# Optimization experiments

Measured on AMD Instinct MI355X. Metric: run time of the kernel, lower is better.

## Reference

```python
import jax, jax.numpy as jnp
import numpy as np

N_NODES = 100000
N_EDGES = 1000000
D_FEAT = 64


def setup_inputs() -> dict:
    key = jax.random.key(0)
    ks = jax.random.split(key, 8)
    X = jax.random.normal(ks[0], (N_NODES, D_FEAT), dtype=jnp.float32)
    ref_a = jax.random.randint(ks[1], (N_EDGES,), 0, N_NODES, dtype=jnp.int32)
    ref_b = jax.random.randint(ks[2], (N_EDGES,), 0, N_NODES, dtype=jnp.int32)
    v_map = jax.random.randint(ks[3], (N_NODES,), 0, 128, dtype=jnp.int32)
    v_count = jax.random.randint(ks[4], (128,), 0, 1000, dtype=jnp.int32)
    # Glorot-uniform weights per build()
    lim = float(np.sqrt(6.0 / (D_FEAT + D_FEAT)))
    W_hidden = jax.random.uniform(ks[5], (D_FEAT, D_FEAT), jnp.float32, -lim, lim)
    W_out = jax.random.uniform(ks[6], (D_FEAT, D_FEAT), jnp.float32, -lim, lim)
    b_hidden = jnp.zeros((D_FEAT,), jnp.float32)
    b_out = jnp.zeros((D_FEAT,), jnp.float32)
    return {
        "X": X, "ref_a": ref_a, "ref_b": ref_b, "v_map": v_map, "v_count": v_count,
        "W_hidden": W_hidden, "b_hidden": b_hidden, "W_out": W_out, "b_out": b_out,
    }


def reference(X, ref_a, ref_b, v_map, v_count, W_hidden, b_hidden, W_out, b_out):
    # gin_convolution_compact: GIN aggregation with eps=0 over a compact
    # (undirected, stored-once) edge list: X_agg[v] = X[v] + sum_{u in N(v)} X[u]
    X_agg = X.at[ref_a].add(X[ref_b])
    X_agg = X_agg.at[ref_b].add(X[ref_a])
    # 2-layer MLP with relu after each layer
    X_hid = jax.nn.relu(X_agg @ W_hidden + b_hidden)
    X_out = jax.nn.relu(X_hid @ W_out + b_out)
    return X_out
```

## Files before the change

### kernel.cpp

```cpp
#include <hip/hip_runtime.h>

#define D_FEAT 64
#define BUK_SHIFT 9
#define NPBUK 512
#define MAX_BUK 256
#define SRC_BITS 20
#define SRC_MASK 0xFFFFFu
#define CHUNK_E 8192
#define MAX_BUK_RECS 16384

__global__ __launch_bounds__(256) void bucket_count_kernel(
    const int* __restrict__ ref_a, const int* __restrict__ ref_b,
    int* __restrict__ buk_cnt, int n_edges) {
    __shared__ int hist[MAX_BUK];
    hist[threadIdx.x] = 0;
    __syncthreads();
    int stride = gridDim.x * blockDim.x;
    for (int e = blockIdx.x * blockDim.x + threadIdx.x; e < n_edges; e += stride) {
        atomicAdd(&hist[ref_a[e] >> BUK_SHIFT], 1);
        atomicAdd(&hist[ref_b[e] >> BUK_SHIFT], 1);
    }
    __syncthreads();
    int c = hist[threadIdx.x];
    if (c) atomicAdd(&buk_cnt[threadIdx.x], c);
}

__global__ void bucket_scan_kernel(int* __restrict__ bs, int* __restrict__ cursor,
                                   int* __restrict__ row_start, int n_nodes) {
    int lane = threadIdx.x;
    int carry = 0;
    for (int base = 0; base < MAX_BUK; base += 64) {
        int i = base + lane;
        int v = bs[i];
        int inc = v;
        #pragma unroll
        for (int d = 1; d < 64; d <<= 1) {
            int t = __shfl_up(inc, d);
            if (lane >= d) inc += t;
        }
        int excl = carry + inc - v;
        bs[i] = excl;
        cursor[i] = excl;
        carry += __shfl(inc, 63);
    }
    if (lane == 0) {
        bs[MAX_BUK] = carry;
        row_start[n_nodes] = carry;
    }
}

__global__ __launch_bounds__(256) void bucket_scatter_kernel(
    const int* __restrict__ ref_a, const int* __restrict__ ref_b,
    int* __restrict__ gcur, unsigned* __restrict__ recs, int n_edges) {
    __shared__ int cnt[MAX_BUK];
    __shared__ int base[MAX_BUK];
    __shared__ int cur[MAX_BUK];
    int tid = threadIdx.x;
    int e0 = blockIdx.x * CHUNK_E;
    int e1 = min(e0 + CHUNK_E, n_edges);

    cnt[tid] = 0;
    __syncthreads();
    for (int e = e0 + tid; e < e1; e += 256) {
        atomicAdd(&cnt[ref_a[e] >> BUK_SHIFT], 1);
        atomicAdd(&cnt[ref_b[e] >> BUK_SHIFT], 1);
    }
    __syncthreads();
    int c = cnt[tid];
    base[tid] = c ? atomicAdd(&gcur[tid], c) : 0;
    cur[tid] = 0;
    __syncthreads();
    for (int e = e0 + tid; e < e1; e += 256) {
        int a = ref_a[e];
        int b = ref_b[e];
        int ba = a >> BUK_SHIFT;
        int pa = base[ba] + atomicAdd(&cur[ba], 1);
        recs[pa] = ((unsigned)(a & (NPBUK - 1)) << SRC_BITS) | (unsigned)b;
        int bb = b >> BUK_SHIFT;
        int pb = base[bb] + atomicAdd(&cur[bb], 1);
        recs[pb] = ((unsigned)(b & (NPBUK - 1)) << SRC_BITS) | (unsigned)a;
    }
}

__global__ __launch_bounds__(256) void bucket_sort_kernel(
    const int* __restrict__ bucket_start,
    unsigned* __restrict__ recs,
    int* __restrict__ row_start, int n_nodes) {
    __shared__ unsigned buf[MAX_BUK_RECS];
    __shared__ int cnt[NPBUK];
    __shared__ int lcur[NPBUK];
    int buk = blockIdx.x;
    int tid = threadIdx.x;
    int s = bucket_start[buk];
    int n = bucket_start[buk + 1] - s;
    for (int i = tid; i < NPBUK; i += 256) cnt[i] = 0;
    __syncthreads();
    for (int i = tid; i < n; i += 256) {
        unsigned r = recs[s + i];
        buf[i] = r;
        atomicAdd(&cnt[r >> SRC_BITS], 1);
    }
    __syncthreads();
    if (tid < 64) {
        int lane = tid;
        int carry = 0;
        for (int b2 = 0; b2 < NPBUK; b2 += 64) {
            int i = b2 + lane;
            int v = cnt[i];
            int inc = v;
            #pragma unroll
            for (int d = 1; d < 64; d <<= 1) {
                int t = __shfl_up(inc, d);
                if (lane >= d) inc += t;
            }
            int excl = carry + inc - v;
            lcur[i] = excl;
            int vg = (buk << BUK_SHIFT) + i;
            if (vg < n_nodes) row_start[vg] = s + excl;
            carry += __shfl(inc, 63);
        }
    }
    __syncthreads();
    for (int i = tid; i < n; i += 256) {
        unsigned r = buf[i];
        int p = atomicAdd(&lcur[r >> SRC_BITS], 1);
        recs[s + p] = r & SRC_MASK;
    }
}

__global__ __launch_bounds__(256) void gather_kernel(
    const float* __restrict__ X,
    const int* __restrict__ row_start,
    const int* __restrict__ adj,
    float* __restrict__ agg, int n_nodes) {
    int gwid = (blockIdx.x * blockDim.x + threadIdx.x) >> 6;
    int j = threadIdx.x & 63;
    if (gwid >= n_nodes) return;
    int v = gwid;
    float acc = X[v * D_FEAT + j];
    int k = row_start[v];
    int kend = row_start[v + 1];
    float a0 = 0.f, a1 = 0.f, a2 = 0.f, a3 = 0.f;
    for (; k + 8 <= kend; k += 8) {
        int u0 = adj[k + 0], u1 = adj[k + 1], u2 = adj[k + 2], u3 = adj[k + 3];
        int u4 = adj[k + 4], u5 = adj[k + 5], u6 = adj[k + 6], u7 = adj[k + 7];
        float r0 = X[u0 * D_FEAT + j], r1 = X[u1 * D_FEAT + j];
        float r2 = X[u2 * D_FEAT + j], r3 = X[u3 * D_FEAT + j];
        float r4 = X[u4 * D_FEAT + j], r5 = X[u5 * D_FEAT + j];
        float r6 = X[u6 * D_FEAT + j], r7 = X[u7 * D_FEAT + j];
        a0 += r0; a1 += r1; a2 += r2; a3 += r3;
        a0 += r4; a1 += r5; a2 += r6; a3 += r7;
    }
    for (; k < kend; ++k) acc += X[adj[k] * D_FEAT + j];
    agg[v * D_FEAT + j] = acc + (a0 + a1) + (a2 + a3);
}

__global__ __launch_bounds__(256) void mlp_kernel(
    float* __restrict__ agg,
    const float* __restrict__ Wh, const float* __restrict__ bh,
    const float* __restrict__ Wo, const float* __restrict__ bo,
    int n_nodes) {
    __shared__ __align__(16) float wh_lds[D_FEAT * D_FEAT];
    __shared__ __align__(16) float wo_lds[D_FEAT * D_FEAT];
    __shared__ __align__(16) float x_lds[4][4][D_FEAT];
    __shared__ __align__(16) float h_lds[4][4][D_FEAT];

    int tid = threadIdx.x;
    {
        const float4* Wh4 = (const float4*)Wh;
        const float4* Wo4 = (const float4*)Wo;
        float4* wh4 = (float4*)wh_lds;
        float4* wo4 = (float4*)wo_lds;
        for (int i = tid; i < D_FEAT * D_FEAT / 4; i += 256) {
            wh4[i] = Wh4[i];
            wo4[i] = Wo4[i];
        }
    }
    int w = tid >> 6;
    int j = tid & 63;
    float bhj = bh[j];
    float boj = bo[j];
    __syncthreads();

    int vbase = blockIdx.x * 16 + w * 4;

    #pragma unroll
    for (int nb = 0; nb < 4; ++nb) {
        int v = vbase + nb;
        x_lds[w][nb][j] = (v < n_nodes) ? agg[v * D_FEAT + j] : 0.0f;
    }

    {
        float a0 = bhj, a1 = bhj, a2 = bhj, a3 = bhj;
        const float4* x0 = (const float4*)x_lds[w][0];
        const float4* x1 = (const float4*)x_lds[w][1];
        const float4* x2 = (const float4*)x_lds[w][2];
        const float4* x3 = (const float4*)x_lds[w][3];
        #pragma unroll
        for (int k4 = 0; k4 < 16; ++k4) {
            float4 p0 = x0[k4], p1 = x1[k4], p2 = x2[k4], p3 = x3[k4];
            float w0 = wh_lds[(k4 * 4 + 0) * D_FEAT + j];
            float w1 = wh_lds[(k4 * 4 + 1) * D_FEAT + j];
            float w2 = wh_lds[(k4 * 4 + 2) * D_FEAT + j];
            float w3 = wh_lds[(k4 * 4 + 3) * D_FEAT + j];
            a0 = fmaf(p0.x, w0, a0); a0 = fmaf(p0.y, w1, a0); a0 = fmaf(p0.z, w2, a0); a0 = fmaf(p0.w, w3, a0);
            a1 = fmaf(p1.x, w0, a1); a1 = fmaf(p1.y, w1, a1); a1 = fmaf(p1.z, w2, a1); a1 = fmaf(p1.w, w3, a1);
            a2 = fmaf(p2.x, w0, a2); a2 = fmaf(p2.y, w1, a2); a2 = fmaf(p2.z, w2, a2); a2 = fmaf(p2.w, w3, a2);
            a3 = fmaf(p3.x, w0, a3); a3 = fmaf(p3.y, w1, a3); a3 = fmaf(p3.z, w2, a3); a3 = fmaf(p3.w, w3, a3);
        }
        h_lds[w][0][j] = fmaxf(a0, 0.0f);
        h_lds[w][1][j] = fmaxf(a1, 0.0f);
        h_lds[w][2][j] = fmaxf(a2, 0.0f);
        h_lds[w][3][j] = fmaxf(a3, 0.0f);
    }

    {
        float a0 = boj, a1 = boj, a2 = boj, a3 = boj;
        const float4* x0 = (const float4*)h_lds[w][0];
        const float4* x1 = (const float4*)h_lds[w][1];
        const float4* x2 = (const float4*)h_lds[w][2];
        const float4* x3 = (const float4*)h_lds[w][3];
        #pragma unroll
        for (int k4 = 0; k4 < 16; ++k4) {
            float4 p0 = x0[k4], p1 = x1[k4], p2 = x2[k4], p3 = x3[k4];
            float w0 = wo_lds[(k4 * 4 + 0) * D_FEAT + j];
            float w1 = wo_lds[(k4 * 4 + 1) * D_FEAT + j];
            float w2 = wo_lds[(k4 * 4 + 2) * D_FEAT + j];
            float w3 = wo_lds[(k4 * 4 + 3) * D_FEAT + j];
            a0 = fmaf(p0.x, w0, a0); a0 = fmaf(p0.y, w1, a0); a0 = fmaf(p0.z, w2, a0); a0 = fmaf(p0.w, w3, a0);
            a1 = fmaf(p1.x, w0, a1); a1 = fmaf(p1.y, w1, a1); a1 = fmaf(p1.z, w2, a1); a1 = fmaf(p1.w, w3, a1);
            a2 = fmaf(p2.x, w0, a2); a2 = fmaf(p2.y, w1, a2); a2 = fmaf(p2.z, w2, a2); a2 = fmaf(p2.w, w3, a2);
            a3 = fmaf(p3.x, w0, a3); a3 = fmaf(p3.y, w1, a3); a3 = fmaf(p3.z, w2, a3); a3 = fmaf(p3.w, w3, a3);
        }
        if (vbase + 0 < n_nodes) agg[(vbase + 0) * D_FEAT + j] = fmaxf(a0, 0.0f);
        if (vbase + 1 < n_nodes) agg[(vbase + 1) * D_FEAT + j] = fmaxf(a1, 0.0f);
        if (vbase + 2 < n_nodes) agg[(vbase + 2) * D_FEAT + j] = fmaxf(a2, 0.0f);
        if (vbase + 3 < n_nodes) agg[(vbase + 3) * D_FEAT + j] = fmaxf(a3, 0.0f);
    }
}

extern "C" void kernel_launch(void* const* d_in, const int* in_sizes, int n_in,
                              void* d_out, int out_size, void* d_ws, size_t ws_size,
                              hipStream_t stream) {
    const float* X     = (const float*)d_in[0];
    const int*   ref_a = (const int*)d_in[1];
    const int*   ref_b = (const int*)d_in[2];
    const float* Wh    = (const float*)d_in[5];
    const float* bh    = (const float*)d_in[6];
    const float* Wo    = (const float*)d_in[7];
    const float* bo    = (const float*)d_in[8];
    float* out = (float*)d_out;

    int n_nodes = in_sizes[0] / D_FEAT;
    int n_edges = in_sizes[1];
    int nbuk = (n_nodes + NPBUK - 1) / NPBUK;

    int* buk_cnt   = (int*)d_ws;
    int* cursor    = buk_cnt + (MAX_BUK + 1);
    int* row_start = cursor + MAX_BUK;
    unsigned* recs = (unsigned*)(row_start + n_nodes + 1);

    hipMemsetAsync(buk_cnt, 0, (MAX_BUK + 1) * sizeof(int), stream);
    bucket_count_kernel<<<256, 256, 0, stream>>>(ref_a, ref_b, buk_cnt, n_edges);
    bucket_scan_kernel<<<1, 64, 0, stream>>>(buk_cnt, cursor, row_start, n_nodes);
    bucket_scatter_kernel<<<(n_edges + CHUNK_E - 1) / CHUNK_E, 256, 0, stream>>>(
        ref_a, ref_b, cursor, recs, n_edges);
    bucket_sort_kernel<<<nbuk, 256, 0, stream>>>(buk_cnt, recs, row_start, n_nodes);

    int gblocks = (n_nodes * 64 + 255) / 256;
    gather_kernel<<<gblocks, 256, 0, stream>>>(X, row_start, (const int*)recs,
                                               out, n_nodes);

    int mblocks = (n_nodes + 15) / 16;
    mlp_kernel<<<mblocks, 256, 0, stream>>>(out, Wh, bh, Wo, bo, n_nodes);
}
```

Baseline: 342.7 us.

## Keep MLP weight columns in registers and use a persistent grid

The MLP kernel now loads each thread's column of both weight matrices into registers once, instead of staging the full matrices in LDS. It runs as a fixed grid of 1024 blocks that loop over node groups, so weight loading is amortized across many groups rather than repeated per block. This removes the per-block LDS weight fill and barrier and frees LDS. The cost is heavy register use (128 weight registers per thread) under a 3-blocks-per-CU launch bound, which may reduce occupancy or cause spills.

Result: slower. 819.5 us (+139.1%).

```diff
diff --git a/kernel.cpp b/kernel.cpp
--- a/kernel.cpp
+++ b/kernel.cpp
@@ -155,87 +155,79 @@
     agg[v * D_FEAT + j] = acc + (a0 + a1) + (a2 + a3);
 }
 
-__global__ __launch_bounds__(256) void mlp_kernel(
+__global__ __launch_bounds__(256, 3) void mlp_kernel(
     float* __restrict__ agg,
     const float* __restrict__ Wh, const float* __restrict__ bh,
     const float* __restrict__ Wo, const float* __restrict__ bo,
     int n_nodes) {
-    __shared__ __align__(16) float wh_lds[D_FEAT * D_FEAT];
-    __shared__ __align__(16) float wo_lds[D_FEAT * D_FEAT];
     __shared__ __align__(16) float x_lds[4][4][D_FEAT];
     __shared__ __align__(16) float h_lds[4][4][D_FEAT];
 
     int tid = threadIdx.x;
-    {
-        const float4* Wh4 = (const float4*)Wh;
-        const float4* Wo4 = (const float4*)Wo;
-        float4* wh4 = (float4*)wh_lds;
-        float4* wo4 = (float4*)wo_lds;
-        for (int i = tid; i < D_FEAT * D_FEAT / 4; i += 256) {
-            wh4[i] = Wh4[i];
-            wo4[i] = Wo4[i];
-        }
-    }
     int w = tid >> 6;
     int j = tid & 63;
+
+    float wh[D_FEAT], wo[D_FEAT];
+    #pragma unroll
+    for (int k = 0; k < D_FEAT; ++k) wh[k] = Wh[k * D_FEAT + j];
+    #pragma unroll
+    for (int k = 0; k < D_FEAT; ++k) wo[k] = Wo[k * D_FEAT + j];
     float bhj = bh[j];
     float boj = bo[j];
-    __syncthreads();
-
-    int vbase = blockIdx.x * 16 + w * 4;
-
-    #pragma unroll
-    for (int nb = 0; nb < 4; ++nb) {
-        int v = vbase + nb;
-        x_lds[w][nb][j] = (v < n_nodes) ? agg[v * D_FEAT + j] : 0.0f;
-    }
-
-    {
+
+    int ngroups = (n_nodes + 15) >> 4;
+    for (int g = blockIdx.x; g < ngroups; g += gridDim.x) {
+        int vbase = g * 16 + w * 4;
+
+        #pragma unroll
+        for (int nb = 0; nb < 4; ++nb) {
+            int v = vbase + nb;
+            x_lds[w][nb][j] = (v < n_nodes) ? agg[v * D_FEAT + j] : 0.0f;
+        }
+
         float a0 = bhj, a1 = bhj, a2 = bhj, a3 = bhj;
-        const float4* x0 = (const float4*)x_lds[w][0];
-        const float4* x1 = (const float4*)x_lds[w][1];
-        const float4* x2 = (const float4*)x_lds[w][2];
-        const float4* x3 = (const float4*)x_lds[w][3];
-        #pragma unroll
-        for (int k4 = 0; k4 < 16; ++k4) {
-            float4 p0 = x0[k4], p1 = x1[k4], p2 = x2[k4], p3 = x3[k4];
-            float w0 = wh_lds[(k4 * 4 + 0) * D_FEAT + j];
-            float w1 = wh_lds[(k4 * 4 + 1) * D_FEAT + j];
-            float w2 = wh_lds[(k4 * 4 + 2) * D_FEAT + j];
-            float w3 = wh_lds[(k4 * 4 + 3) * D_FEAT + j];
-            a0 = fmaf(p0.x, w0, a0); a0 = fmaf(p0.y, w1, a0); a0 = fmaf(p0.z, w2, a0); a0 = fmaf(p0.w, w3, a0);
-            a1 = fmaf(p1.x, w0, a1); a1 = fmaf(p1.y, w1, a1); a1 = fmaf(p1.z, w2, a1); a1 = fmaf(p1.w, w3, a1);
-            a2 = fmaf(p2.x, w0, a2); a2 = fmaf(p2.y, w1, a2); a2 = fmaf(p2.z, w2, a2); a2 = fmaf(p2.w, w3, a2);
-            a3 = fmaf(p3.x, w0, a3); a3 = fmaf(p3.y, w1, a3); a3 = fmaf(p3.z, w2, a3); a3 = fmaf(p3.w, w3, a3);
+        {
+            const float4* x0 = (const float4*)x_lds[w][0];
+            const float4* x1 = (const float4*)x_lds[w][1];
+            const float4* x2 = (const float4*)x_lds[w][2];
+            const float4* x3 = (const float4*)x_lds[w][3];
+            #pragma unroll
+            for (int k4 = 0; k4 < 16; ++k4) {
+                float4 p0 = x0[k4], p1 = x1[k4], p2 = x2[k4], p3 = x3[k4];
+                float w0 = wh[k4 * 4 + 0], w1 = wh[k4 * 4 + 1];
+                float w2 = wh[k4 * 4 + 2], w3 = wh[k4 * 4 + 3];
+                a0 = fmaf(p0.x, w0, a0); a0 = fmaf(p0.y, w1, a0); a0 = fmaf(p0.z, w2, a0); a0 = fmaf(p0.w, w3, a0);
+                a1 = fmaf(p1.x, w0, a1); a1 = fmaf(p1.y, w1, a1); a1 = fmaf(p1.z, w2, a1); a1 = fmaf(p1.w, w3, a1);
+                a2 = fmaf(p2.x, w0, a2); a2 = fmaf(p2.y, w1, a2); a2 = fmaf(p2.z, w2, a2); a2 = fmaf(p2.w, w3, a2);
+                a3 = fmaf(p3.x, w0, a3); a3 = fmaf(p3.y, w1, a3); a3 = fmaf(p3.z, w2, a3); a3 = fmaf(p3.w, w3, a3);
+            }
         }
         h_lds[w][0][j] = fmaxf(a0, 0.0f);
         h_lds[w][1][j] = fmaxf(a1, 0.0f);
         h_lds[w][2][j] = fmaxf(a2, 0.0f);
         h_lds[w][3][j] = fmaxf(a3, 0.0f);
-    }
-
-    {
-        float a0 = boj, a1 = boj, a2 = boj, a3 = boj;
-        const float4* x0 = (const float4*)h_lds[w][0];
-        const float4* x1 = (const float4*)h_lds[w][1];
-        const float4* x2 = (const float4*)h_lds[w][2];
-        const float4* x3 = (const float4*)h_lds[w][3];
-        #pragma unroll
-        for (int k4 = 0; k4 < 16; ++k4) {
-            float4 p0 = x0[k4], p1 = x1[k4], p2 = x2[k4], p3 = x3[k4];
-            float w0 = wo_lds[(k4 * 4 + 0) * D_FEAT + j];
-            float w1 = wo_lds[(k4 * 4 + 1) * D_FEAT + j];
-            float w2 = wo_lds[(k4 * 4 + 2) * D_FEAT + j];
-            float w3 = wo_lds[(k4 * 4 + 3) * D_FEAT + j];
-            a0 = fmaf(p0.x, w0, a0); a0 = fmaf(p0.y, w1, a0); a0 = fmaf(p0.z, w2, a0); a0 = fmaf(p0.w, w3, a0);
-            a1 = fmaf(p1.x, w0, a1); a1 = fmaf(p1.y, w1, a1); a1 = fmaf(p1.z, w2, a1); a1 = fmaf(p1.w, w3, a1);
-            a2 = fmaf(p2.x, w0, a2); a2 = fmaf(p2.y, w1, a2); a2 = fmaf(p2.z, w2, a2); a2 = fmaf(p2.w, w3, a2);
-            a3 = fmaf(p3.x, w0, a3); a3 = fmaf(p3.y, w1, a3); a3 = fmaf(p3.z, w2, a3); a3 = fmaf(p3.w, w3, a3);
-        }
-        if (vbase + 0 < n_nodes) agg[(vbase + 0) * D_FEAT + j] = fmaxf(a0, 0.0f);
-        if (vbase + 1 < n_nodes) agg[(vbase + 1) * D_FEAT + j] = fmaxf(a1, 0.0f);
-        if (vbase + 2 < n_nodes) agg[(vbase + 2) * D_FEAT + j] = fmaxf(a2, 0.0f);
-        if (vbase + 3 < n_nodes) agg[(vbase + 3) * D_FEAT + j] = fmaxf(a3, 0.0f);
+
+        float c0 = boj, c1 = boj, c2 = boj, c3 = boj;
+        {
+            const float4* x0 = (const float4*)h_lds[w][0];
+            const float4* x1 = (const float4*)h_lds[w][1];
+            const float4* x2 = (const float4*)h_lds[w][2];
+            const float4* x3 = (const float4*)h_lds[w][3];
+            #pragma unroll
+            for (int k4 = 0; k4 < 16; ++k4) {
+                float4 p0 = x0[k4], p1 = x1[k4], p2 = x2[k4], p3 = x3[k4];
+                float w0 = wo[k4 * 4 + 0], w1 = wo[k4 * 4 + 1];
+                float w2 = wo[k4 * 4 + 2], w3 = wo[k4 * 4 + 3];
+                c0 = fmaf(p0.x, w0, c0); c0 = fmaf(p0.y, w1, c0); c0 = fmaf(p0.z, w2, c0); c0 = fmaf(p0.w, w3, c0);
+                c1 = fmaf(p1.x, w0, c1); c1 = fmaf(p1.y, w1, c1); c1 = fmaf(p1.z, w2, c1); c1 = fmaf(p1.w, w3, c1);
+                c2 = fmaf(p2.x, w0, c2); c2 = fmaf(p2.y, w1, c2); c2 = fmaf(p2.z, w2, c2); c2 = fmaf(p2.w, w3, c2);
+                c3 = fmaf(p3.x, w0, c3); c3 = fmaf(p3.y, w1, c3); c3 = fmaf(p3.z, w2, c3); c3 = fmaf(p3.w, w3, c3);
+            }
+        }
+        if (vbase + 0 < n_nodes) agg[(vbase + 0) * D_FEAT + j] = fmaxf(c0, 0.0f);
+        if (vbase + 1 < n_nodes) agg[(vbase + 1) * D_FEAT + j] = fmaxf(c1, 0.0f);
+        if (vbase + 2 < n_nodes) agg[(vbase + 2) * D_FEAT + j] = fmaxf(c2, 0.0f);
+        if (vbase + 3 < n_nodes) agg[(vbase + 3) * D_FEAT + j] = fmaxf(c3, 0.0f);
     }
 }
 
@@ -271,6 +263,5 @@
     gather_kernel<<<gblocks, 256, 0, stream>>>(X, row_start, (const int*)recs,
                                                out, n_nodes);
 
-    int mblocks = (n_nodes + 15) / 16;
-    mlp_kernel<<<mblocks, 256, 0, stream>>>(out, Wh, bh, Wo, bo, n_nodes);
-}
+    mlp_kernel<<<1024, 256, 0, stream>>>(out, Wh, bh, Wo, bo, n_nodes);
+}
```
